# Optimization experiments

Measured on AMD Instinct MI355X. Metric: run time of the kernel, lower is better.

The kernel has to match this reference:

```python
import jax, jax.numpy as jnp
import numpy as np
from jax import lax

N, L, K, DROP = 2048, 512, 16, 2
DIM = N - L * DROP  # 1024 father wavelets


def setup_inputs() -> dict:
    key = jax.random.key(0)
    kA, kO = jax.random.split(key)
    A = jax.random.normal(kA, (N, N), dtype=jnp.float32)
    A = 0.5 * (A + A.T)  # symmetric, like a graph Laplacian
    O = jax.random.normal(kO, (L, K, K), dtype=jnp.float32) / np.float32(np.sqrt(K))
    # Index structure faithful to the module: each level selects K indices,
    # DROP of which are freshly-dropped wavelet indices, the rest drawn from
    # the pool of indices that stay active through all L levels.
    rng = np.random.default_rng(0)
    perm = rng.permutation(N)
    dropped = perm[: L * DROP].reshape(L, DROP)
    pool = perm[L * DROP:]  # size DIM, always active
    rest = np.stack([rng.choice(pool, K - DROP, replace=False) for _ in range(L)])
    idx = np.sort(np.concatenate([dropped, rest], axis=1), axis=1).astype(np.int32)
    active_idx = np.sort(pool).astype(np.int32)        # final_active_index == 1
    inactive_idx = np.sort(perm[: L * DROP]).astype(np.int32)  # dropped (mother)
    return {
        "A": A,
        "O": O,
        "idx": jnp.asarray(idx),
        "active_idx": jnp.asarray(active_idx),
        "inactive_idx": jnp.asarray(inactive_idx),
    }


def reference(A, O, idx, active_idx, inactive_idx):
    n = A.shape[0]
    dt = A.dtype

    # Each level's U is identity except the KxK block O at rows/cols idx[l].
    # Hence U @ A @ U^T only rewrites K rows then K cols of A, and U @ right
    # only rewrites K rows of right -- same math as the dense NxN matmuls in
    # the original, expressed as the O(N*K) structured update.
    def step(carry, xs):
        Acur, right = carry
        Ol, il = xs
        Acur = Acur.at[il].set(Ol @ Acur[il])              # rows of U @ A
        Acur = Acur.at[:, il].set(Acur[:, il] @ Ol.T)      # cols of (U@A) @ U^T
        right = right.at[il].set(Ol @ right[il])           # U @ right
        return (Acur, right), None

    right0 = jnp.eye(n, dtype=dt)  # right after l==0 becomes U_0 @ I = U_0
    (A_out, right), _ = lax.scan(step, (A, right0), (O, idx))

    active = jnp.zeros((n,), dt).at[active_idx].set(1.0)
    outer = active[:, None] * active[None, :]
    # left_index = I - diag(diag(outer)) + outer ; diag(outer) == active
    left = jnp.eye(n, dtype=dt) - jnp.diag(active) + outer
    D = A_out * left

    mother_coefficients = D[jnp.ix_(inactive_idx, inactive_idx)]  # (N-dim, N-dim)
    father_coefficients = D[jnp.ix_(active_idx, active_idx)]      # (dim, dim)
    mother_wavelets = right[inactive_idx]                         # (N-dim, N)
    father_wavelets = right[active_idx]                           # (dim, N)
    A_rec = right.T @ D @ right
    return (A_rec, right, D, mother_coefficients, father_coefficients,
            mother_wavelets, father_wavelets)
```

## Files before the change

### kernel.cpp

```cpp
#include <hip/hip_runtime.h>

#define NDIM 2048
#define LLEV 512
#define KDIM 16
#define HALF 1024

typedef __attribute__((ext_vector_type(8))) short bf16x8;
typedef __attribute__((ext_vector_type(4))) float f32x4;

__device__ inline unsigned short f2bf(float x) {
    unsigned u = __float_as_uint(x);
    u += 0x7fffu + ((u >> 16) & 1u);
    return (unsigned short)(u >> 16);
}
__device__ inline float bf2f(unsigned short b) {
    return __uint_as_float(((unsigned)b) << 16);
}
__device__ inline void split2(float x, unsigned short& h, unsigned short& l) {
    h = f2bf(x);
    l = f2bf(x - bf2f(h));
}

__device__ inline void gl2lds16(const void* g, void* l) {
    __builtin_amdgcn_global_load_lds(
        (const __attribute__((address_space(1))) void*)g,
        (__attribute__((address_space(3))) void*)l, 16, 0, 0);
}

__global__ __launch_bounds__(64) void compose_kernel(const float* __restrict__ O,
                                                     const int* __restrict__ idx,
                                                     int* __restrict__ Sarr,
                                                     float* __restrict__ Warr)
{
    __shared__ int s_S[32];
    __shared__ int s_pos[32];
    __shared__ float s_W[32][33];
    const int t = blockIdx.x;
    const int lane = threadIdx.x;
    const int* a = idx + (2 * t) * 16;
    const int* b = idx + (2 * t + 1) * 16;

    if (lane == 0) {
        int na = 0, i = 0, j = 0;
        while (i < 16 || j < 16) {
            int va = (i < 16) ? a[i] : 0x7fffffff;
            int vb = (j < 16) ? b[j] : 0x7fffffff;
            int v = va < vb ? va : vb;
            if (va == v) i++;
            if (vb == v) j++;
            s_S[na++] = v;
        }
        const int nm = na;
        int r = 0, p = 0;
        while (na < 32) {
            while (p < nm && s_S[p] < r) p++;
            if (p < nm && s_S[p] == r) { r++; continue; }
            s_S[na++] = r++;
        }
    }
    __syncthreads();
    if (lane < 32) {
        const int v = (lane < 16) ? a[lane] : b[lane - 16];
        int pp = 0;
        #pragma unroll
        for (int q = 0; q < 32; ++q) if (s_S[q] == v) pp = q;
        s_pos[lane] = pp;
        #pragma unroll
        for (int c = 0; c < 33; ++c) s_W[lane][c] = 0.f;
        s_W[lane][lane] = 1.f;
    }
    __syncthreads();
    const int j  = lane >> 2;
    const int cg = (lane & 3) * 8;
    #pragma unroll
    for (int step = 0; step < 2; ++step) {
        const float* Om = O + (size_t)(2 * t + step) * 256;
        float acc[8] = {};
        for (int k = 0; k < 16; ++k) {
            const float o = Om[j * 16 + k];
            const int p = s_pos[step * 16 + k];
            #pragma unroll
            for (int c = 0; c < 8; ++c) acc[c] += o * s_W[p][cg + c];
        }
        __syncthreads();
        const int pj = s_pos[step * 16 + j];
        #pragma unroll
        for (int c = 0; c < 8; ++c) s_W[pj][cg + c] = acc[c];
        __syncthreads();
    }
    if (lane < 32) Sarr[t * 32 + lane] = s_S[lane];
    {
        const int r = lane >> 1, h0 = (lane & 1) * 16;
        float* wp = Warr + (size_t)t * 1024 + r * 32 + h0;
        #pragma unroll
        for (int c = 0; c < 16; ++c) wp[c] = s_W[r][h0 + c];
    }
}

__global__ __launch_bounds__(64) void scan3_kernel(const float* __restrict__ Warr,
                                                   const int* __restrict__ Sarr,
                                                   float* __restrict__ right)
{
    __shared__ float slab[NDIM * 4];
    const int lane = threadIdx.x;
    const int c0 = blockIdx.x * 4;
    const int rr = lane & 31;
    const int ks = lane >> 5;

    for (int r = lane; r < NDIM; r += 64)
        *(float4*)&slab[r * 4] = make_float4(0.f, 0.f, 0.f, 0.f);
    if (lane < 4) slab[(c0 + lane) * 4 + lane] = 1.0f;

    int rows[16]; float cf[16]; int wrow;
    {
        const int4* sp = (const int4*)(Sarr + ks * 16);
        #pragma unroll
        for (int q = 0; q < 4; ++q) *(int4*)&rows[q * 4] = sp[q];
        const float4* wp = (const float4*)(Warr + rr * 32 + ks * 16);
        #pragma unroll
        for (int q = 0; q < 4; ++q) *(float4*)&cf[q * 4] = wp[q];
        wrow = Sarr[rr];
    }

    for (int t = 0; t < 256; ++t) {
        int cr[16]; float cc[16];
        const int wr = wrow;
        #pragma unroll
        for (int q = 0; q < 16; ++q) { cr[q] = rows[q]; cc[q] = cf[q]; }
        if (t + 1 < 256) {
            const int4* sp = (const int4*)(Sarr + (t + 1) * 32 + ks * 16);
            #pragma unroll
            for (int q = 0; q < 4; ++q) *(int4*)&rows[q * 4] = sp[q];
            const float4* wp = (const float4*)(Warr + (size_t)(t + 1) * 1024 + rr * 32 + ks * 16);
            #pragma unroll
            for (int q = 0; q < 4; ++q) *(float4*)&cf[q * 4] = wp[q];
            wrow = Sarr[(t + 1) * 32 + rr];
        }
        float4 acc = make_float4(0.f, 0.f, 0.f, 0.f);
        #pragma unroll
        for (int j = 0; j < 16; ++j) {
            float4 v = *(const float4*)&slab[cr[j] * 4];
            acc.x += cc[j] * v.x; acc.y += cc[j] * v.y;
            acc.z += cc[j] * v.z; acc.w += cc[j] * v.w;
        }
        acc.x += __shfl_xor(acc.x, 32, 64);
        acc.y += __shfl_xor(acc.y, 32, 64);
        acc.z += __shfl_xor(acc.z, 32, 64);
        acc.w += __shfl_xor(acc.w, 32, 64);
        if (lane < 32)
            *(float4*)&slab[wr * 4] = acc;
    }

    #pragma unroll 4
    for (int i = 0; i < 32; ++i) {
        const int r = i * 64 + lane;
        *(float4*)(right + (size_t)r * NDIM + c0) = *(float4*)&slab[r * 4];
    }
}

__global__ __launch_bounds__(64) void scan_kernel(const float* __restrict__ O,
                                                  const int* __restrict__ idx,
                                                  float* __restrict__ right)
{
    __shared__ float slab[NDIM * 8];
    const int lane = threadIdx.x;
    const int c0 = blockIdx.x * 8;
    const int k  = lane >> 2;
    const int c2 = (lane & 3) * 2;

    for (int r = lane; r < NDIM; r += 64) {
        *(float4*)&slab[r * 8]     = make_float4(0.f, 0.f, 0.f, 0.f);
        *(float4*)&slab[r * 8 + 4] = make_float4(0.f, 0.f, 0.f, 0.f);
    }
    if (lane < 8) slab[(c0 + lane) * 8 + lane] = 1.0f;

    int rows[16]; float a[16]; int wrow;
    #pragma unroll
    for (int j = 0; j < 16; ++j) rows[j] = idx[j];
    {
        const float4* p4 = (const float4*)(O + k * 16);
        #pragma unroll
        for (int q = 0; q < 4; ++q) *(float4*)&a[q * 4] = p4[q];
    }
    wrow = idx[k];

    for (int l = 0; l < LLEV; ++l) {
        int rr[16]; float aa[16];
        const int wr = wrow;
        #pragma unroll
        for (int j = 0; j < 16; ++j) { rr[j] = rows[j]; aa[j] = a[j]; }
        if (l + 1 < LLEV) {
            const int* ip = idx + (l + 1) * 16;
            #pragma unroll
            for (int j = 0; j < 16; ++j) rows[j] = ip[j];
            const float4* p4 = (const float4*)(O + (l + 1) * 256 + k * 16);
            #pragma unroll
            for (int q = 0; q < 4; ++q) *(float4*)&a[q * 4] = p4[q];
            wrow = ip[k];
        }
        float sx = 0.f, sy = 0.f;
        #pragma unroll
        for (int j = 0; j < 16; ++j) {
            float2 v = *(float2*)&slab[rr[j] * 8 + c2];
            sx += aa[j] * v.x;
            sy += aa[j] * v.y;
        }
        *(float2*)&slab[wr * 8 + c2] = make_float2(sx, sy);
    }

    for (int r0 = 0; r0 < NDIM; r0 += 32) {
        const int r = r0 + (lane >> 1);
        const int h = (lane & 1) * 4;
        *(float4*)(right + (size_t)r * NDIM + c0 + h) = *(float4*)&slab[r * 8 + h];
    }
}

#define GBK 64
__global__ __launch_bounds__(256) void mfma_nt(const unsigned short* __restrict__ Ah,
                                               const unsigned short* __restrict__ Al,
                                               const unsigned short* __restrict__ Bh,
                                               const unsigned short* __restrict__ Bl,
                                               float* __restrict__ C,
                                               long strideZ,
                                               int M, int N, int K, int ksplit)
{
    __shared__ unsigned short sA_h[8 * 128 * 8];
    __shared__ unsigned short sA_l[8 * 128 * 8];
    __shared__ unsigned short sB_h[8 * 128 * 8];
    __shared__ unsigned short sB_l[8 * 128 * 8];

    const int tid  = threadIdx.x;
    const int wave = tid >> 6, lane = tid & 63;
    const int lm   = lane & 15, quad = lane >> 4;
    const int wm   = wave & 1,  wn   = wave >> 1;
    const int m0   = blockIdx.x * 128, n0 = blockIdx.y * 128;
    const int Kz   = K / ksplit;
    const int kbeg = Kz * blockIdx.z;
    C += (size_t)blockIdx.z * strideZ;

    const unsigned short* gbase;
    unsigned short* sbase;
    if      (wave == 0) { gbase = Ah + (size_t)m0 * K; sbase = sA_h; }
    else if (wave == 1) { gbase = Al + (size_t)m0 * K; sbase = sA_l; }
    else if (wave == 2) { gbase = Bh + (size_t)n0 * K; sbase = sB_h; }
    else                { gbase = Bl + (size_t)n0 * K; sbase = sB_l; }

    f32x4 acc[4][4];
    #pragma unroll
    for (int i = 0; i < 4; ++i)
        #pragma unroll
        for (int j = 0; j < 4; ++j) acc[i][j] = (f32x4){0.f, 0.f, 0.f, 0.f};

    for (int k0 = kbeg; k0 < kbeg + Kz; k0 += GBK) {
        #pragma unroll
        for (int h = 0; h < 2; ++h) {
            const unsigned short* gr = gbase + (size_t)(h * 64 + lane) * K + k0;
            unsigned short* sb = sbase + h * 512;
            #pragma unroll
            for (int c = 0; c < 8; ++c)
                gl2lds16(gr + c * 8, sb + c * 1024);
        }
        __syncthreads();
        #pragma unroll
        for (int sub = 0; sub < 2; ++sub) {
            const int co = (sub * 4 + quad) * 1024;
            bf16x8 ah[4], al[4], bh[4], bl[4];
            #pragma unroll
            for (int i = 0; i < 4; ++i) {
                const int m = wm * 64 + i * 16 + lm;
                ah[i] = *(const bf16x8*)&sA_h[co + m * 8];
                al[i] = *(const bf16x8*)&sA_l[co + m * 8];
            }
            #pragma unroll
            for (int j = 0; j < 4; ++j) {
                const int n = wn * 64 + j * 16 + lm;
                bh[j] = *(const bf16x8*)&sB_h[co + n * 8];
                bl[j] = *(const bf16x8*)&sB_l[co + n * 8];
            }
            #pragma unroll
            for (int i = 0; i < 4; ++i)
                #pragma unroll
                for (int j = 0; j < 4; ++j) {
                    acc[i][j] = __builtin_amdgcn_mfma_f32_16x16x32_bf16(ah[i], bh[j], acc[i][j], 0, 0, 0);
                    acc[i][j] = __builtin_amdgcn_mfma_f32_16x16x32_bf16(ah[i], bl[j], acc[i][j], 0, 0, 0);
                    acc[i][j] = __builtin_amdgcn_mfma_f32_16x16x32_bf16(al[i], bh[j], acc[i][j], 0, 0, 0);
                }
        }
        __syncthreads();
    }
    #pragma unroll
    for (int i = 0; i < 4; ++i) {
        const int mrow = m0 + wm * 64 + i * 16 + quad * 4;
        #pragma unroll
        for (int j = 0; j < 4; ++j) {
            float* cp = C + (size_t)mrow * N + n0 + wn * 64 + j * 16 + lm;
            #pragma unroll
            for (int r = 0; r < 4; ++r) cp[(size_t)r * N] = acc[i][j][r];
        }
    }
}

__global__ __launch_bounds__(256) void reduce_k(float* __restrict__ dst,
                                                const float* __restrict__ parts,
                                                long strideZ, int nz, long n)
{
    const long i = ((long)blockIdx.x * 256 + threadIdx.x) * 4;
    if (i >= n) return;
    float4 s = *(const float4*)(parts + i);
    for (int z = 1; z < nz; ++z) {
        float4 v = *(const float4*)(parts + (size_t)z * strideZ + i);
        s.x += v.x; s.y += v.y; s.z += v.z; s.w += v.w;
    }
    *(float4*)(dst + i) = s;
}

__global__ __launch_bounds__(256) void conv_hl(const float* __restrict__ src,
                                               const int* __restrict__ gidx,
                                               int kshift,
                                               unsigned short* __restrict__ h,
                                               unsigned short* __restrict__ l)
{
    const long e = ((long)blockIdx.x * 256 + threadIdx.x) * 4;
    const float* s;
    if (gidx) {
        const long row = e >> kshift;
        const long col = e - (row << kshift);
        s = src + ((size_t)gidx[row] << kshift) + col;
    } else {
        s = src + e;
    }
    float4 v = *(const float4*)s;
    ushort4 hh, ll;
    split2(v.x, hh.x, ll.x); split2(v.y, hh.y, ll.y);
    split2(v.z, hh.z, ll.z); split2(v.w, hh.w, ll.w);
    *(ushort4*)(h + e) = hh;
    *(ushort4*)(l + e) = ll;
}

__global__ __launch_bounds__(256) void tconv_hl(const float* __restrict__ src,
                                                int Msrc, int Ksrc,
                                                unsigned short* __restrict__ h,
                                                unsigned short* __restrict__ l)
{
    __shared__ float t[64][65];
    const int bi = blockIdx.x, bj = blockIdx.y;
    const int tx = threadIdx.x & 15, ty = threadIdx.x >> 4;
    #pragma unroll
    for (int r = 0; r < 4; ++r) {
        const int row = bi * 64 + ty + r * 16;
        float4 v = *(const float4*)(src + (size_t)row * Ksrc + bj * 64 + tx * 4);
        t[ty + r * 16][tx * 4 + 0] = v.x; t[ty + r * 16][tx * 4 + 1] = v.y;
        t[ty + r * 16][tx * 4 + 2] = v.z; t[ty + r * 16][tx * 4 + 3] = v.w;
    }
    __syncthreads();
    #pragma unroll
    for (int r = 0; r < 4; ++r) {
        const int drow = bj * 64 + ty + r * 16;
        ushort4 hh, ll;
        split2(t[tx * 4 + 0][ty + r * 16], hh.x, ll.x);
        split2(t[tx * 4 + 1][ty + r * 16], hh.y, ll.y);
        split2(t[tx * 4 + 2][ty + r * 16], hh.z, ll.z);
        split2(t[tx * 4 + 3][ty + r * 16], hh.w, ll.w);
        *(ushort4*)(h + (size_t)drow * Msrc + bi * 64 + tx * 4) = hh;
        *(ushort4*)(l + (size_t)drow * Msrc + bi * 64 + tx * 4) = ll;
    }
}

__global__ __launch_bounds__(256) void gt_build(const float* __restrict__ W1,
                                                const float* __restrict__ right,
                                                const int* __restrict__ inva,
                                                const float* __restrict__ dmrow,
                                                unsigned short* __restrict__ h,
                                                unsigned short* __restrict__ l)
{
    __shared__ float t[64][65];
    const int bi = blockIdx.x, bj = blockIdx.y;
    const int tx = threadIdx.x & 15, ty = threadIdx.x >> 4;
    #pragma unroll
    for (int rr = 0; rr < 4; ++rr) {
        const int r = bi * 64 + ty + rr * 16;
        const int ia = inva[r];
        float4 v;
        if (ia >= 0) {
            v = *(const float4*)(W1 + (size_t)ia * NDIM + bj * 64 + tx * 4);
        } else {
            v = *(const float4*)(right + (size_t)r * NDIM + bj * 64 + tx * 4);
            const float s = dmrow[r];
            v.x *= s; v.y *= s; v.z *= s; v.w *= s;
        }
        t[ty + rr * 16][tx * 4 + 0] = v.x; t[ty + rr * 16][tx * 4 + 1] = v.y;
        t[ty + rr * 16][tx * 4 + 2] = v.z; t[ty + rr * 16][tx * 4 + 3] = v.w;
    }
    __syncthreads();
    #pragma unroll
    for (int rr = 0; rr < 4; ++rr) {
        const int drow = bj * 64 + ty + rr * 16;
        ushort4 hh, ll;
        split2(t[tx * 4 + 0][ty + rr * 16], hh.x, ll.x);
        split2(t[tx * 4 + 1][ty + rr * 16], hh.y, ll.y);
        split2(t[tx * 4 + 2][ty + rr * 16], hh.z, ll.z);
        split2(t[tx * 4 + 3][ty + rr * 16], hh.w, ll.w);
        *(ushort4*)(h + (size_t)drow * NDIM + bi * 64 + tx * 4) = hh;
        *(ushort4*)(l + (size_t)drow * NDIM + bi * 64 + tx * 4) = ll;
    }
}

__global__ __launch_bounds__(256) void diag_kernel(const float* __restrict__ P,
                                                   const float* __restrict__ R,
                                                   float* __restrict__ diag_all)
{
    __shared__ float red[256];
    const int i = blockIdx.x;
    const float4* p4 = (const float4*)(P + (size_t)i * NDIM);
    const float4* r4 = (const float4*)(R + (size_t)i * NDIM);
    float s = 0.f;
    for (int kq = threadIdx.x; kq < NDIM / 4; kq += 256) {
        float4 a = p4[kq], b = r4[kq];
        s += a.x * b.x + a.y * b.y + a.z * b.z + a.w * b.w;
    }
    red[threadIdx.x] = s;
    __syncthreads();
    for (int off = 128; off > 0; off >>= 1) {
        if (threadIdx.x < off) red[threadIdx.x] += red[threadIdx.x + off];
        __syncthreads();
    }
    if (threadIdx.x == 0) diag_all[i] = red[0];
}

__global__ void prep2_kernel(const int* __restrict__ act, const int* __restrict__ inact,
                             const float* __restrict__ diag_all,
                             int* __restrict__ inva, float* __restrict__ dm,
                             float* __restrict__ dmrow)
{
    const int t = threadIdx.x;
    inva[t] = -1;
    inva[t + HALF] = -1;
    __syncthreads();
    inva[act[t]] = t;
    const int ir = inact[t];
    const float dv = diag_all[ir];
    dm[t] = dv;
    dmrow[ir] = dv;
}

__global__ __launch_bounds__(256) void build_D(const float* __restrict__ Daa,
                                               const float* __restrict__ diag_all,
                                               const int* __restrict__ inva,
                                               float* __restrict__ D)
{
    const int e = blockIdx.x * 256 + threadIdx.x;
    const int i = e >> 11, j = e & (NDIM - 1);
    const int ii = inva[i], jj = inva[j];
    float v = 0.f;
    if (ii >= 0 && jj >= 0) v = Daa[ii * HALF + jj];
    if (i == j) v = diag_all[i];
    D[e] = v;
}

__global__ __launch_bounds__(256) void mc_kernel(const float* __restrict__ dm,
                                                 float* __restrict__ mc)
{
    const int e = blockIdx.x * 256 + threadIdx.x;
    const int t = e >> 10, s = e & (HALF - 1);
    mc[e] = (t == s) ? dm[t] : 0.f;
}

__global__ __launch_bounds__(512) void gather_rows(const float* __restrict__ R,
                                                   const int* __restrict__ ridx,
                                                   float* __restrict__ outp)
{
    const int r = blockIdx.x;
    const int c = threadIdx.x * 4;
    *(float4*)(outp + (size_t)r * NDIM + c) =
        *(const float4*)(R + (size_t)ridx[r] * NDIM + c);
}

__global__ __launch_bounds__(256) void gemm_nt64(const float* __restrict__ A, int lda,
                                                 const int* __restrict__ ridxA,
                                                 const float* __restrict__ B, int ldb,
                                                 const int* __restrict__ ridxB,
                                                 float* __restrict__ C, int ldc, int Kk)
{
    __shared__ float As[16][68];
    __shared__ float Bs[16][68];
    const int tid = threadIdx.x;
    const int tx = tid & 15, ty = tid >> 4;
    const int m0 = blockIdx.x * 64, n0 = blockIdx.y * 64;
    const int li = tid >> 2;
    const int lk = (tid & 3) * 4;
    int rowA = m0 + li; if (ridxA) rowA = ridxA[rowA];
    int rowB = n0 + li; if (ridxB) rowB = ridxB[rowB];
    const float* pA = A + (size_t)rowA * lda + lk;
    const float* pB = B + (size_t)rowB * ldb + lk;
    float acc[4][4] = {};
    for (int k0 = 0; k0 < Kk; k0 += 16) {
        float4 a4 = *(const float4*)(pA + k0);
        float4 b4 = *(const float4*)(pB + k0);
        As[lk + 0][li] = a4.x; As[lk + 1][li] = a4.y; As[lk + 2][li] = a4.z; As[lk + 3][li] = a4.w;
        Bs[lk + 0][li] = b4.x; Bs[lk + 1][li] = b4.y; Bs[lk + 2][li] = b4.z; Bs[lk + 3][li] = b4.w;
        __syncthreads();
        #pragma unroll
        for (int kk = 0; kk < 16; ++kk) {
            float4 av = *(const float4*)&As[kk][ty * 4];
            float4 bv = *(const float4*)&Bs[kk][tx * 4];
            float a[4] = {av.x, av.y, av.z, av.w};
            float b[4] = {bv.x, bv.y, bv.z, bv.w};
            #pragma unroll
            for (int i = 0; i < 4; ++i)
                #pragma unroll
                for (int j = 0; j < 4; ++j) acc[i][j] += a[i] * b[j];
        }
        __syncthreads();
    }
    #pragma unroll
    for (int i = 0; i < 4; ++i) {
        float4 v = make_float4(acc[i][0], acc[i][1], acc[i][2], acc[i][3]);
        *(float4*)(C + (size_t)(m0 + ty * 4 + i) * ldc + n0 + tx * 4) = v;
    }
}

__global__ __launch_bounds__(256) void gemm_nn64(const float* __restrict__ A, int lda,
                                                 const float* __restrict__ B, int ldb,
                                                 float* __restrict__ C, int ldc, int Kk)
{
    __shared__ float As[16][68];
    __shared__ float Bs[16][68];
    const int tid = threadIdx.x;
    const int tx = tid & 15, ty = tid >> 4;
    const int m0 = blockIdx.x * 64, n0 = blockIdx.y * 64;
    const int li = tid >> 2;
    const int lk = (tid & 3) * 4;
    const int bk = tid >> 4;
    const int bn = (tid & 15) * 4;
    const float* pA = A + (size_t)(m0 + li) * lda + lk;
    float acc[4][4] = {};
    for (int k0 = 0; k0 < Kk; k0 += 16) {
        float4 a4 = *(const float4*)(pA + k0);
        float4 b4 = *(const float4*)(B + (size_t)(k0 + bk) * ldb + n0 + bn);
        As[lk + 0][li] = a4.x; As[lk + 1][li] = a4.y; As[lk + 2][li] = a4.z; As[lk + 3][li] = a4.w;
        *(float4*)&Bs[bk][bn] = b4;
        __syncthreads();
        #pragma unroll
        for (int kk = 0; kk < 16; ++kk) {
            float4 av = *(const float4*)&As[kk][ty * 4];
            float4 bv = *(const float4*)&Bs[kk][tx * 4];
            float a[4] = {av.x, av.y, av.z, av.w};
            float b[4] = {bv.x, bv.y, bv.z, bv.w};
            #pragma unroll
            for (int i = 0; i < 4; ++i)
                #pragma unroll
                for (int j = 0; j < 4; ++j) acc[i][j] += a[i] * b[j];
        }
        __syncthreads();
    }
    #pragma unroll
    for (int i = 0; i < 4; ++i) {
        float4 v = make_float4(acc[i][0], acc[i][1], acc[i][2], acc[i][3]);
        *(float4*)(C + (size_t)(m0 + ty * 4 + i) * ldc + n0 + tx * 4) = v;
    }
}

__global__ __launch_bounds__(256) void arec64(const float* __restrict__ fw,
                                              const float* __restrict__ mw,
                                              const float* __restrict__ W1,
                                              const float* __restrict__ dm,
                                              float* __restrict__ C)
{
    __shared__ float As[16][68];
    __shared__ float Bs[16][68];
    const int tid = threadIdx.x;
    const int tx = tid & 15, ty = tid >> 4;
    const int m0 = blockIdx.x * 64, n0 = blockIdx.y * 64;
    const int bk = tid >> 4;
    const int bn = (tid & 15) * 4;
    float acc[4][4] = {};
    for (int t0 = 0; t0 < NDIM; t0 += 16) {
        const int t = t0 + bk;
        const float* Hrow; const float* Grow; float gs;
        if (t < HALF) { Hrow = fw + (size_t)t * NDIM; Grow = W1 + (size_t)t * NDIM; gs = 1.f; }
        else          { Hrow = mw + (size_t)(t - HALF) * NDIM; Grow = Hrow; gs = dm[t - HALF]; }
        float4 a4 = *(const float4*)(Hrow + m0 + bn);
        float4 b4 = *(const float4*)(Grow + n0 + bn);
        b4.x *= gs; b4.y *= gs; b4.z *= gs; b4.w *= gs;
        *(float4*)&As[bk][bn] = a4;
        *(float4*)&Bs[bk][bn] = b4;
        __syncthreads();
        #pragma unroll
        for (int kk = 0; kk < 16; ++kk) {
            float4 av = *(const float4*)&As[kk][ty * 4];
            float4 bv = *(const float4*)&Bs[kk][tx * 4];
            float a[4] = {av.x, av.y, av.z, av.w};
            float b[4] = {bv.x, bv.y, bv.z, bv.w};
            #pragma unroll
            for (int i = 0; i < 4; ++i)
                #pragma unroll
                for (int j = 0; j < 4; ++j) acc[i][j] += a[i] * b[j];
        }
        __syncthreads();
    }
    #pragma unroll
    for (int i = 0; i < 4; ++i) {
        float4 v = make_float4(acc[i][0], acc[i][1], acc[i][2], acc[i][3]);
        *(float4*)(C + (size_t)(m0 + ty * 4 + i) * NDIM + n0 + tx * 4) = v;
    }
}

extern "C" void kernel_launch(void* const* d_in, const int* in_sizes, int n_in,
                              void* d_out, int out_size, void* d_ws, size_t ws_size,
                              hipStream_t stream)
{
    (void)in_sizes; (void)n_in; (void)out_size;
    const float* A     = (const float*)d_in[0];
    const float* O     = (const float*)d_in[1];
    const int*   idx   = (const int*)d_in[2];
    const int*   act   = (const int*)d_in[3];
    const int*   inact = (const int*)d_in[4];

    float* out = (float*)d_out;
    const size_t NN = (size_t)NDIM * NDIM;
    float* A_rec = out;
    float* right = out + NN;
    float* D     = out + 2 * NN;
    float* mc    = out + 3 * NN;
    float* fc    = mc + (size_t)HALF * HALF;
    float* mw    = fc + (size_t)HALF * HALF;
    float* fw    = mw + (size_t)HALF * NDIM;

    char*  w        = (char*)d_ws;
    float* diag_all = (float*)w;
    float* dm       = (float*)(w + 8192);
    int*   inva     = (int*)(w + 12288);
    float* dmrow    = (float*)(w + 20480);

    const size_t MB = 1024 * 1024;
    const size_t WS_NEEDED = 65536 + 32 * MB;

    if (ws_size >= WS_NEEDED) {
        char* r1 = w + 65536;
        char* r2 = r1 + 16 * MB;
        float* Warr = (float*)r1;
        int*   Sarr = (int*)(r1 + MB);
        unsigned short* Rh  = (unsigned short*)r1;
        unsigned short* Rl  = (unsigned short*)(r1 + 8 * MB);
        unsigned short* RTh = Rh;
        unsigned short* RTl = Rl;
        unsigned short* Ah  = (unsigned short*)r2;
        unsigned short* Al  = (unsigned short*)(r2 + 8 * MB);
        unsigned short* Pah = (unsigned short*)r2;
        unsigned short* Pal = (unsigned short*)(r2 + 4 * MB);
        unsigned short* Fh  = (unsigned short*)(r2 + 8 * MB);
        unsigned short* Fl  = (unsigned short*)(r2 + 12 * MB);
        unsigned short* Dh  = (unsigned short*)r2;
        unsigned short* Dl  = (unsigned short*)(r2 + 2 * MB);
        unsigned short* FTh = (unsigned short*)(r2 + 4 * MB);
        unsigned short* FTl = (unsigned short*)(r2 + 8 * MB);
        unsigned short* GTh = (unsigned short*)r2;
        unsigned short* GTl = (unsigned short*)(r2 + 8 * MB);

        compose_kernel<<<256, 64, 0, stream>>>(O, idx, Sarr, Warr);
        scan3_kernel<<<512, 64, 0, stream>>>(Warr, Sarr, right);
        gather_rows<<<1024, 512, 0, stream>>>(right, act, fw);
        gather_rows<<<1024, 512, 0, stream>>>(right, inact, mw);
        conv_hl<<<4096, 256, 0, stream>>>(right, nullptr, 11, Rh, Rl);
        conv_hl<<<4096, 256, 0, stream>>>(A, nullptr, 11, Ah, Al);
        mfma_nt<<<dim3(16, 16, 2), 256, 0, stream>>>(Rh, Rl, Ah, Al, A_rec,
                                                     (long)2 * NN, NDIM, NDIM, NDIM, 2);
        reduce_k<<<4096, 256, 0, stream>>>(A_rec, A_rec, (long)2 * NN, 2, (long)NN);
        diag_kernel<<<2048, 256, 0, stream>>>(A_rec, right, diag_all);
        prep2_kernel<<<1, 1024, 0, stream>>>(act, inact, diag_all, inva, dm, dmrow);
        conv_hl<<<2048, 256, 0, stream>>>(A_rec, act, 11, Pah, Pal);
        conv_hl<<<2048, 256, 0, stream>>>(fw, nullptr, 11, Fh, Fl);
        mfma_nt<<<dim3(8, 8, 4), 256, 0, stream>>>(Pah, Pal, Fh, Fl, D,
                                                   (long)HALF * HALF, HALF, HALF, NDIM, 4);
        reduce_k<<<1024, 256, 0, stream>>>(fc, D, (long)HALF * HALF, 4, (long)HALF * HALF);
        conv_hl<<<1024, 256, 0, stream>>>(fc, nullptr, 10, Dh, Dl);
        tconv_hl<<<dim3(16, 32), 256, 0, stream>>>(fw, HALF, NDIM, FTh, FTl);
        mfma_nt<<<dim3(8, 16, 2), 256, 0, stream>>>(Dh, Dl, FTh, FTl, D,
                                                    (long)HALF * NDIM, HALF, NDIM, HALF, 2);
        reduce_k<<<2048, 256, 0, stream>>>(D, D, (long)HALF * NDIM, 2, (long)HALF * NDIM);
        tconv_hl<<<dim3(32, 32), 256, 0, stream>>>(right, NDIM, NDIM, RTh, RTl);
        gt_build<<<dim3(32, 32), 256, 0, stream>>>(D, right, inva, dmrow, GTh, GTl);
        mfma_nt<<<dim3(16, 16, 2), 256, 0, stream>>>(RTh, RTl, GTh, GTl, A_rec,
                                                     (long)2 * NN, NDIM, NDIM, NDIM, 2);
        reduce_k<<<4096, 256, 0, stream>>>(A_rec, A_rec, (long)2 * NN, 2, (long)NN);
        build_D<<<16384, 256, 0, stream>>>(fc, diag_all, inva, D);
        mc_kernel<<<4096, 256, 0, stream>>>(dm, mc);
    } else {
        scan_kernel<<<256, 64, 0, stream>>>(O, idx, right);
        gather_rows<<<1024, 512, 0, stream>>>(right, act, fw);
        gather_rows<<<1024, 512, 0, stream>>>(right, inact, mw);
        gemm_nt64<<<dim3(32, 32), 256, 0, stream>>>(right, NDIM, nullptr, A, NDIM, nullptr,
                                                    A_rec, NDIM, NDIM);
        diag_kernel<<<2048, 256, 0, stream>>>(A_rec, right, diag_all);
        prep2_kernel<<<1, 1024, 0, stream>>>(act, inact, diag_all, inva, dm, dmrow);
        gemm_nt64<<<dim3(16, 16), 256, 0, stream>>>(A_rec, NDIM, act, right, NDIM, act,
                                                    fc, HALF, NDIM);
        gemm_nn64<<<dim3(16, 32), 256, 0, stream>>>(fc, HALF, fw, NDIM, D, NDIM, HALF);
        arec64<<<dim3(32, 32), 256, 0, stream>>>(fw, mw, D, dm, A_rec);
        build_D<<<16384, 256, 0, stream>>>(fc, diag_all, inva, D);
        mc_kernel<<<4096, 256, 0, stream>>>(dm, mc);
    }
}
```

Baseline: 570.0 us.

## Compose adjacent level pairs into 64x64 blocks to halve sequential scan steps

Adds a compose2 kernel that merges each pair of 32-wide composed transforms into one 64-wide block matrix over the union of their indices. The right-matrix scan then runs 128 sequential steps instead of 256, with each lane owning one output row so the cross-half shuffle reduction goes away. It also packs the row byte offsets as 16-bit pairs and double-buffers coefficient loads across steps. The aim is a shorter serial dependency chain in the scan, paid for with more FLOPs per step, an extra kernel launch and higher register pressure from the 64-float coefficient buffers.

```diff
diff --git a/kernel.cpp b/kernel.cpp
--- a/kernel.cpp
+++ b/kernel.cpp
@@ -7,6 +7,7 @@
 
 typedef __attribute__((ext_vector_type(8))) short bf16x8;
 typedef __attribute__((ext_vector_type(4))) float f32x4;
+typedef __attribute__((ext_vector_type(2))) float f32x2;
 
 __device__ inline unsigned short f2bf(float x) {
     unsigned u = __float_as_uint(x);
@@ -97,59 +98,158 @@
     }
 }
 
-__global__ __launch_bounds__(64) void scan3_kernel(const float* __restrict__ Warr,
-                                                   const int* __restrict__ Sarr,
+__global__ __launch_bounds__(64) void compose2_kernel(const float* __restrict__ Warr,
+                                                      const int* __restrict__ Sarr,
+                                                      float* __restrict__ Warr2,
+                                                      int* __restrict__ Sarr2,
+                                                      unsigned int* __restrict__ Spk)
+{
+    __shared__ int s_S[64];
+    __shared__ int s_pos[64];
+    __shared__ unsigned s_map[64];
+    __shared__ float s_W[64][68];
+    const int t = blockIdx.x;
+    const int lane = threadIdx.x;
+    const int* a = Sarr + (2 * t) * 32;
+    const int* b = Sarr + (2 * t + 1) * 32;
+
+    s_map[lane] = 0u;
+    __syncthreads();
+    if (lane == 0) {
+        int na = 0;
+        for (int k = 0; k < 32; ++k) {
+            const int v = a[k];
+            s_map[v >> 5] |= 1u << (v & 31);
+            s_S[na++] = v;
+        }
+        for (int k = 0; k < 32; ++k) {
+            const int v = b[k];
+            if (!((s_map[v >> 5] >> (v & 31)) & 1u)) {
+                s_map[v >> 5] |= 1u << (v & 31);
+                s_S[na++] = v;
+            }
+        }
+        int r = 0;
+        while (na < 64) {
+            if (!((s_map[r >> 5] >> (r & 31)) & 1u)) s_S[na++] = r;
+            ++r;
+        }
+    }
+    __syncthreads();
+    {
+        const int v = (lane < 32) ? a[lane] : b[lane - 32];
+        int pp = 0;
+        for (int q = 0; q < 64; ++q) if (s_S[q] == v) pp = q;
+        s_pos[lane] = pp;
+        #pragma unroll
+        for (int c = 0; c < 68; ++c) s_W[lane][c] = 0.f;
+        s_W[lane][lane] = 1.f;
+    }
+    __syncthreads();
+    const int j  = lane >> 1;
+    const int cg = (lane & 1) * 32;
+    #pragma unroll
+    for (int step = 0; step < 2; ++step) {
+        const float* Om = Warr + (size_t)(2 * t + step) * 1024 + j * 32;
+        float acc[32] = {};
+        for (int k = 0; k < 32; ++k) {
+            const float o = Om[k];
+            const int p = s_pos[step * 32 + k];
+            #pragma unroll
+            for (int c4 = 0; c4 < 8; ++c4) {
+                float4 v = *(const float4*)&s_W[p][cg + c4 * 4];
+                acc[c4 * 4 + 0] += o * v.x;
+                acc[c4 * 4 + 1] += o * v.y;
+                acc[c4 * 4 + 2] += o * v.z;
+                acc[c4 * 4 + 3] += o * v.w;
+            }
+        }
+        __syncthreads();
+        const int pj = s_pos[step * 32 + j];
+        #pragma unroll
+        for (int c4 = 0; c4 < 8; ++c4) {
+            float4 v = make_float4(acc[c4 * 4 + 0], acc[c4 * 4 + 1],
+                                   acc[c4 * 4 + 2], acc[c4 * 4 + 3]);
+            *(float4*)&s_W[pj][cg + c4 * 4] = v;
+        }
+        __syncthreads();
+    }
+    Sarr2[t * 64 + lane] = s_S[lane];
+    if (lane < 32)
+        Spk[t * 32 + lane] = (unsigned)(s_S[2 * lane] << 4)
+                           | ((unsigned)(s_S[2 * lane + 1] << 4) << 16);
+    {
+        float* wp = Warr2 + (size_t)t * 4096 + lane * 64;
+        #pragma unroll
+        for (int c = 0; c < 16; ++c)
+            *(float4*)&wp[c * 4] = *(const float4*)&s_W[lane][c * 4];
+    }
+}
+
+__global__ __launch_bounds__(64) void scan4_kernel(const float* __restrict__ Warr2,
+                                                   const int* __restrict__ Sarr2,
+                                                   const unsigned int* __restrict__ Spk,
                                                    float* __restrict__ right)
 {
     __shared__ float slab[NDIM * 4];
     const int lane = threadIdx.x;
     const int c0 = blockIdx.x * 4;
-    const int rr = lane & 31;
-    const int ks = lane >> 5;
 
     for (int r = lane; r < NDIM; r += 64)
         *(float4*)&slab[r * 4] = make_float4(0.f, 0.f, 0.f, 0.f);
     if (lane < 4) slab[(c0 + lane) * 4 + lane] = 1.0f;
 
-    int rows[16]; float cf[16]; int wrow;
-    {
-        const int4* sp = (const int4*)(Sarr + ks * 16);
-        #pragma unroll
-        for (int q = 0; q < 4; ++q) *(int4*)&rows[q * 4] = sp[q];
-        const float4* wp = (const float4*)(Warr + rr * 32 + ks * 16);
-        #pragma unroll
-        for (int q = 0; q < 4; ++q) *(float4*)&cf[q * 4] = wp[q];
-        wrow = Sarr[rr];
-    }
-
-    for (int t = 0; t < 256; ++t) {
-        int cr[16]; float cc[16];
-        const int wr = wrow;
-        #pragma unroll
-        for (int q = 0; q < 16; ++q) { cr[q] = rows[q]; cc[q] = cf[q]; }
-        if (t + 1 < 256) {
-            const int4* sp = (const int4*)(Sarr + (t + 1) * 32 + ks * 16);
-            #pragma unroll
-            for (int q = 0; q < 4; ++q) *(int4*)&rows[q * 4] = sp[q];
-            const float4* wp = (const float4*)(Warr + (size_t)(t + 1) * 1024 + rr * 32 + ks * 16);
-            #pragma unroll
-            for (int q = 0; q < 4; ++q) *(float4*)&cf[q * 4] = wp[q];
-            wrow = Sarr[(t + 1) * 32 + rr];
-        }
-        float4 acc = make_float4(0.f, 0.f, 0.f, 0.f);
-        #pragma unroll
-        for (int j = 0; j < 16; ++j) {
-            float4 v = *(const float4*)&slab[cr[j] * 4];
-            acc.x += cc[j] * v.x; acc.y += cc[j] * v.y;
-            acc.z += cc[j] * v.z; acc.w += cc[j] * v.w;
-        }
-        acc.x += __shfl_xor(acc.x, 32, 64);
-        acc.y += __shfl_xor(acc.y, 32, 64);
-        acc.z += __shfl_xor(acc.z, 32, 64);
-        acc.w += __shfl_xor(acc.w, 32, 64);
-        if (lane < 32)
-            *(float4*)&slab[wr * 4] = acc;
-    }
+#define LOADSTEP(PK, CF, WB, tt)                                              \
+    {                                                                         \
+        const int4* sp_ = (const int4*)(Spk + (size_t)(tt) * 32);             \
+        _Pragma("unroll")                                                     \
+        for (int q = 0; q < 8; ++q) PK[q] = sp_[q];                           \
+        const float4* wp_ = (const float4*)(Warr2 + (size_t)(tt) * 4096 + lane * 64); \
+        _Pragma("unroll")                                                     \
+        for (int q = 0; q < 16; ++q) *(float4*)&CF[q * 4] = wp_[q];           \
+        WB = Sarr2[(size_t)(tt) * 64 + lane] << 4;                            \
+    }
+
+#define PROC(WORD, C0, C1)                                                    \
+    {                                                                         \
+        const unsigned w_ = (unsigned)(WORD);                                 \
+        float4 v0_ = *(const float4*)((const char*)slab + (w_ & 0xffffu));    \
+        float4 v1_ = *(const float4*)((const char*)slab + (w_ >> 16));        \
+        const f32x2 cc0_ = {(C0), (C0)};                                      \
+        const f32x2 cc1_ = {(C1), (C1)};                                      \
+        a0 += ((f32x2){v0_.x, v0_.y}) * cc0_;                                 \
+        a1 += ((f32x2){v0_.z, v0_.w}) * cc0_;                                 \
+        a0 += ((f32x2){v1_.x, v1_.y}) * cc1_;                                 \
+        a1 += ((f32x2){v1_.z, v1_.w}) * cc1_;                                 \
+    }
+
+#define COMPSTEP(PK, CF, WB)                                                  \
+    {                                                                         \
+        f32x2 a0 = {0.f, 0.f}, a1 = {0.f, 0.f};                              \
+        _Pragma("unroll")                                                     \
+        for (int q = 0; q < 8; ++q) {                                         \
+            PROC(PK[q].x, CF[q * 8 + 0], CF[q * 8 + 1])                       \
+            PROC(PK[q].y, CF[q * 8 + 2], CF[q * 8 + 3])                       \
+            PROC(PK[q].z, CF[q * 8 + 4], CF[q * 8 + 5])                       \
+            PROC(PK[q].w, CF[q * 8 + 6], CF[q * 8 + 7])                       \
+        }                                                                     \
+        float4 out_ = make_float4(a0.x, a0.y, a1.x, a1.y);                    \
+        *(float4*)((char*)slab + (WB)) = out_;                                \
+    }
+
+    int4 pkA[8]; float cfA[64]; int wbA;
+    int4 pkB[8]; float cfB[64]; int wbB;
+    LOADSTEP(pkA, cfA, wbA, 0)
+    for (int t = 0; t < 128; t += 2) {
+        LOADSTEP(pkB, cfB, wbB, t + 1)
+        COMPSTEP(pkA, cfA, wbA)
+        if (t + 2 < 128) LOADSTEP(pkA, cfA, wbA, t + 2)
+        COMPSTEP(pkB, cfB, wbB)
+    }
+
+#undef LOADSTEP
+#undef PROC
+#undef COMPSTEP
 
     #pragma unroll 4
     for (int i = 0; i < 32; ++i) {
@@ -638,8 +738,11 @@
     if (ws_size >= WS_NEEDED) {
         char* r1 = w + 65536;
         char* r2 = r1 + 16 * MB;
-        float* Warr = (float*)r1;
-        int*   Sarr = (int*)(r1 + MB);
+        float* Warr  = (float*)r1;
+        int*   Sarr  = (int*)(r1 + MB);
+        float* Warr2 = (float*)(r1 + 2 * MB);
+        int*   Sarr2 = (int*)(r1 + 4 * MB);
+        unsigned* Spk = (unsigned*)(r1 + 4 * MB + 32 * 1024);
         unsigned short* Rh  = (unsigned short*)r1;
         unsigned short* Rl  = (unsigned short*)(r1 + 8 * MB);
         unsigned short* RTh = Rh;
@@ -658,7 +761,8 @@
         unsigned short* GTl = (unsigned short*)(r2 + 8 * MB);
 
         compose_kernel<<<256, 64, 0, stream>>>(O, idx, Sarr, Warr);
-        scan3_kernel<<<512, 64, 0, stream>>>(Warr, Sarr, right);
+        compose2_kernel<<<128, 64, 0, stream>>>(Warr, Sarr, Warr2, Sarr2, Spk);
+        scan4_kernel<<<512, 64, 0, stream>>>(Warr2, Sarr2, Spk, right);
         gather_rows<<<1024, 512, 0, stream>>>(right, act, fw);
         gather_rows<<<1024, 512, 0, stream>>>(right, inact, mw);
         conv_hl<<<4096, 256, 0, stream>>>(right, nullptr, 11, Rh, Rl);
```

Result: slower. 699.3 us (+22.7%).
